# Kernel optimization log

Hardware: AMD Instinct MI355X
Metric: run time of the kernel (lower is better)

The kernel has to match this reference:

```python
import jax, jax.numpy as jnp
import numpy as np

THRESHOLD = 0.5  # default threshold from MemoryPool.update

N, D, P, C0 = 16384, 1024, 4096, 2048


def setup_inputs() -> dict:
    key = jax.random.key(0)
    k1, k2, k3, k4 = jax.random.split(key, 4)
    summaries = jax.random.normal(k1, (N, D), dtype=jnp.float32)
    scores = jax.random.uniform(k2, (N,), dtype=jnp.float32)
    slot = jnp.arange(P)
    # slots >= count are empty (zeros), matching fresh torch buffers
    pool = jnp.where((slot < C0)[:, None],
                     jax.random.normal(k3, (P, D), dtype=jnp.float32), 0.0)
    priorities = jnp.where(slot < C0,
                           jax.random.uniform(k4, (P,), dtype=jnp.float32), 0.0)
    return {"summaries": summaries, "scores": scores,
            "pool": pool, "priorities": priorities, "count": C0}


def reference(summaries, scores, pool, priorities, count):
    pool_size = pool.shape[0]
    cnt0 = jnp.asarray(count, jnp.int32)

    def step(carry, xc):
        pl, pr, cnt = carry
        s, sc = xc  # (D,), ()
        valid = sc > THRESHOLD
        min_idx = jnp.argmin(pr)
        has_room = cnt < pool_size
        idx = jnp.where(has_room, cnt, min_idx)
        replace_ok = sc > pr[min_idx]
        do_write = valid & (has_room | replace_ok)
        new_pl = jnp.where(do_write, pl.at[idx].set(s), pl)
        new_pr = jnp.where(do_write, pr.at[idx].set(sc), pr)
        new_cnt = cnt + (do_write & has_room).astype(jnp.int32)
        return (new_pl, new_pr, new_cnt), None

    (pool_out, prior_out, cnt_out), _ = jax.lax.scan(
        step, (pool, priorities, cnt0), (summaries, scores))
    return pool_out, prior_out, cnt_out
```

## Files before the change

### kernel.cpp

```cpp
#include <hip/hip_runtime.h>

typedef unsigned long long u64;
#define THRESH 0.5f
#define ALL1 0xFFFFFFFFFFFFFFFFull
#define FINF __builtin_inff()

__device__ __forceinline__ u64 shflxU64(u64 v, int m) { return __shfl_xor(v, m, 64); }
__device__ __forceinline__ void sort64(u64 &key, int lane) {
#pragma unroll
    for (int k = 2; k <= 64; k <<= 1) {
#pragma unroll
        for (int j = k >> 1; j > 0; j >>= 1) {
            u64 p = shflxU64(key, j);
            bool takeMax = ((lane & j) != 0) != ((lane & k) != 0);
            u64 mn = key < p ? key : p;
            u64 mx = key < p ? p : key;
            key = takeMax ? mx : mn;
        }
    }
}

__device__ __forceinline__ u64 mkey(float v, int id) {
    v = (v == 0.0f) ? 0.0f : v;
    unsigned u = __float_as_uint(v);
    u ^= (unsigned)((int)u >> 31) | 0x80000000u;
    return ((u64)u << 32) | (unsigned)id;
}

__global__ __launch_bounds__(1024) void k1_scan(
    const float* __restrict__ scores, const float* __restrict__ priorities,
    const int* __restrict__ countPtr, int N, int P,
    float* __restrict__ outPrior, float* __restrict__ outCnt, int* __restrict__ srcWs,
    float* __restrict__ cval, int* __restrict__ csrc, int* __restrict__ meta)
{
    const int tid = threadIdx.x;
    for (int s = tid; s < P; s += 1024) { outPrior[s] = priorities[s]; srcWs[s] = -1; }
    int C0 = *countPtr; C0 = C0 < 0 ? 0 : (C0 > P ? P : C0);
    const int per = (N + 1023) >> 10;
    const int i0 = tid * per;
    float sv[16];
    if (per == 16 && i0 + 16 <= N) {
        const float4* s4 = (const float4*)(scores + i0);
        const float4 a = s4[0], b = s4[1], c4 = s4[2], d = s4[3];
        sv[0]=a.x; sv[1]=a.y; sv[2]=a.z; sv[3]=a.w;
        sv[4]=b.x; sv[5]=b.y; sv[6]=b.z; sv[7]=b.w;
        sv[8]=c4.x; sv[9]=c4.y; sv[10]=c4.z; sv[11]=c4.w;
        sv[12]=d.x; sv[13]=d.y; sv[14]=d.z; sv[15]=d.w;
    } else {
#pragma unroll 16
        for (int j = 0; j < 16; ++j)
            sv[j] = (j < per && i0 + j < N) ? scores[i0 + j] : 0.f;
    }
    int c = 0;
#pragma unroll 16
    for (int j = 0; j < 16; ++j) c += (j < per && i0 + j < N && sv[j] > THRESH) ? 1 : 0;
    __shared__ int sb[1024];
    sb[tid] = c; __syncthreads();
    for (int off = 1; off < 1024; off <<= 1) {
        int v = (tid >= off) ? sb[tid - off] : 0;
        __syncthreads();
        sb[tid] += v;
        __syncthreads();
    }
    const int total = sb[1023];
    int v = sb[tid] - c;
    int A = P - C0; if (A > total) A = total; if (A < 0) A = 0;
#pragma unroll 16
    for (int j = 0; j < 16; ++j) {
        if (j < per && i0 + j < N) {
            const float sc = sv[j];
            if (sc > THRESH) {
                if (v < A) { outPrior[C0 + v] = sc; srcWs[C0 + v] = i0 + j; }
                else { cval[v - A] = sc; csrc[v - A] = i0 + j; }
                ++v;
            }
        }
    }
    if (tid == 0) {
        meta[0] = total - A;
        meta[1] = C0 + A;
        outCnt[0] = (float)(C0 + A);
    }
}

#define K2T 512
__global__ __launch_bounds__(256) void k2_count(
    const float* __restrict__ outPrior, const float* __restrict__ cval,
    const int* __restrict__ meta, int* __restrict__ cnt2)
{
    const int M = meta[0], F = meta[1];
    const int iB = blockIdx.x << 8;
    if (iB >= M) return;
    const int hi = min(M, iB + 256);
    const int smax = F + hi;
    const int tb = blockIdx.y * K2T;
    if (tb >= smax) return;
    const int te = min(smax - tb, K2T);
    __shared__ __align__(16) float tile[K2T];
    for (int t = threadIdx.x; t < K2T; t += 256) {
        const int s = tb + t;
        tile[t] = (t < te) ? ((s < F) ? outPrior[s] : cval[s - F]) : FINF;
    }
    __syncthreads();
    const int i = iB + threadIdx.x;
    if (i >= M) return;
    const float x = cval[i];
    int cnt = 0;
    const float4* t4 = (const float4*)tile;
    if (tb + K2T <= F + iB) {
#pragma unroll 8
        for (int q = 0; q < K2T / 4; ++q) {
            const float4 w = t4[q];
            cnt += (w.x < x) + (w.y < x) + (w.z < x) + (w.w < x);
        }
    } else {
        int lim = F + i - tb;
        if (lim < 0) lim = 0;
        if (lim > te) lim = te;
        const int l4 = lim >> 2;
        for (int q = 0; q < l4; ++q) {
            const float4 w = t4[q];
            cnt += (w.x < x) + (w.y < x) + (w.z < x) + (w.w < x);
        }
        for (int t = l4 << 2; t < lim; ++t) cnt += tile[t] < x;
    }
    if (cnt) atomicAdd(&cnt2[i], cnt);
}

__global__ __launch_bounds__(1024) void k3_compact(
    const float* __restrict__ cval, const int* __restrict__ csrc,
    const int* __restrict__ cnt2, int* __restrict__ meta,
    float* __restrict__ cvalS, float* __restrict__ wval, int* __restrict__ wsrc,
    int* __restrict__ writeNum)
{
    const int M = meta[0];
    const int tid = threadIdx.x;
    const int per = (M + 1023) >> 10;
    const int i0 = tid * per, i1 = min(i0 + per, M);
    int c = 0;
    for (int i = i0; i < i1; ++i) c += (cnt2[i] >= i + 1) ? 1 : 0;
    __shared__ int sb[1024];
    sb[tid] = c; __syncthreads();
    for (int off = 1; off < 1024; off <<= 1) {
        int v = (tid >= off) ? sb[tid - off] : 0;
        __syncthreads();
        sb[tid] += v;
        __syncthreads();
    }
    int w = sb[tid] - c;
    for (int i = i0; i < i1; ++i) {
        if (cnt2[i] >= i + 1) {
            wval[w] = cval[i]; wsrc[w] = csrc[i]; writeNum[i] = w; cvalS[i] = cval[i]; ++w;
        } else { writeNum[i] = -1; cvalS[i] = FINF; }
    }
    if (tid == 0) meta[2] = sb[1023];
}

#define K4T 512
__global__ __launch_bounds__(256) void k4_count(
    const float* __restrict__ outPrior, const float* __restrict__ cvalS,
    const int* __restrict__ meta, int P, int* __restrict__ cnt4)
{
    const int M = meta[0], F = meta[1];
    if (M == 0) return;
    const int tot = F + M;
    const int eB = blockIdx.x << 8;
    if (eB >= tot) return;
    const int tb = blockIdx.y * K4T;
    if (tb >= tot) return;
    const int te = min(tot - tb, K4T);
    __shared__ __align__(16) u64 tile[K4T];
    for (int t = threadIdx.x; t < K4T; t += 256) {
        const int s = tb + t;
        u64 kk = ALL1;
        if (t < te) {
            if (s < F) kk = mkey(outPrior[s], s);
            else       kk = mkey(cvalS[s - F], P + (s - F));
        }
        tile[t] = kk;
    }
    __syncthreads();
    const int e = eB + threadIdx.x;
    if (e >= tot) return;
    float x; int id;
    if (e < F) { x = outPrior[e]; id = e; }
    else {
        x = cvalS[e - F];
        if (x == FINF) return;
        id = P + (e - F);
    }
    const u64 kx = mkey(x, id);
    int cnt = 0;
    const ulonglong2* t2 = (const ulonglong2*)tile;
#pragma unroll 8
    for (int q = 0; q < K4T / 2; ++q) {
        const ulonglong2 w = t2[q];
        cnt += (int)(w.x < kx) + (int)(w.y < kx);
    }
    if (cnt) atomicAdd(&cnt4[e], cnt);
}

__global__ __launch_bounds__(256) void k4_scatter(
    const float* __restrict__ outPrior, const float* __restrict__ cvalS,
    const int* __restrict__ writeNum, const int* __restrict__ meta, int P,
    const int* __restrict__ cnt4,
    float* __restrict__ evV, int* __restrict__ evId, int* __restrict__ survW)
{
    const int M = meta[0], F = meta[1], R = meta[2];
    if (M == 0) return;
    const int tot = F + M;
    const int e = blockIdx.x * 256 + threadIdx.x;
    if (e >= tot) return;
    float x; int myid; bool isCand = false; int wn = -1;
    if (e < F) { x = outPrior[e]; myid = e; }
    else {
        const int i = e - F;
        x = cvalS[i];
        if (x == FINF) return;
        isCand = true; wn = writeNum[i]; myid = P + i;
    }
    const int cnt = cnt4[e];
    if (isCand) survW[wn] = (cnt >= R) ? 1 : 0;
    if (cnt < R + 64) { evV[cnt] = x; evId[cnt] = isCand ? (P + wn) : myid; }
}

#define SCAP 14400
#define DONEF (1 << 30)
#define MSF   (1 << 29)
#define TIEF  (1 << 28)
#define RSF   (1 << 27)
#define PAYM  ((1 << 27) - 1)
__global__ __launch_bounds__(1024) void k5_chain(
    const float* __restrict__ evV, const int* __restrict__ evId,
    const int* __restrict__ meta, int P,
    const float* __restrict__ wval, const int* __restrict__ wsrc,
    int* __restrict__ survW,
    float* __restrict__ outPrior, int* __restrict__ srcWs)
{
    __shared__ int state[SCAP];
    __shared__ int shRp, shLeft;
    const int tid = threadIdx.x;
    const int R = meta[2];
    if (R <= 0 || R > SCAP) return;
    const int F = meta[1];
    const int Wtot = F + R;

    if (tid == 0) {
        int Rp = R;
        if (R < Wtot) {
            const float vR1 = evV[R - 1];
            if (evV[R] == vR1) {
                int rr = R - 1;
                while (rr >= 0 && evV[rr] == vR1) --rr;
                Rp = rr + 1;
            }
        }
        shRp = Rp;
    }
    __syncthreads();
    const int Rp = shRp;

    for (int r = tid; r < Rp; r += 1024) {
        const float v = evV[r];
        const bool tp = (r > 0) && (evV[r - 1] == v);
        const bool tn = (r + 1 < Rp) && (evV[r + 1] == v);
        const bool tie = tp || tn;
        const int rs = (tie && !tp) ? RSF : 0;
        const int id = evId[r];
        int st;
        if (id < P) st = id | MSF | (tie ? (TIEF | rs) : DONEF);
        else        st = (id - P) | (tie ? (TIEF | rs) : 0);
        state[r] = st;
    }
    __syncthreads();

    for (int round = 0; round < Rp + 2; ++round) {
        for (int r = tid; r < Rp; r += 1024) {
            const int s = state[r];
            if (s & MSF) continue;
            int p = s & PAYM;
            int ms = -1;
            for (int g = 0; g < Rp + 2; ++g) {
                const int sp = state[p];
                if (sp & DONEF) { ms = sp & PAYM; break; }
                if (sp & (MSF | TIEF)) break;
                const int q = sp & PAYM;
                if (q >= p) break;
                p = q;
            }
            if (ms >= 0)
                state[r] = ms | MSF | ((s & TIEF) ? (s & (TIEF | RSF)) : DONEF);
            else
                state[r] = p | (s & (TIEF | RSF));
        }
        __syncthreads();
        for (int r = tid; r < Rp; r += 1024) {
            const int s = state[r];
            if (!(s & RSF) || (s & DONEF)) continue;
            int re = r + 1;
            while (re < Rp) {
                const int t = state[re];
                if ((t & TIEF) && !(t & RSF)) ++re; else break;
            }
            bool ready = true;
            for (int q = r; q < re; ++q) ready &= (state[q] & MSF) != 0;
            if (!ready) continue;
            for (int j = r; j < re; ++j) {
                int best = j;
                for (int q = j + 1; q < re; ++q)
                    if ((state[q] & PAYM) < (state[best] & PAYM)) best = q;
                if (best != j) {
                    const int pj = state[j] & PAYM, pb = state[best] & PAYM;
                    state[j]    = (state[j] & ~PAYM) | pb;
                    state[best] = (state[best] & ~PAYM) | pj;
                }
            }
            for (int j = r; j < re; ++j) state[j] |= DONEF;
        }
        __syncthreads();
        if (tid == 0) shLeft = 0;
        __syncthreads();
        int loc = 0;
        for (int r = tid; r < Rp; r += 1024) loc += (state[r] & DONEF) ? 0 : 1;
        if (loc) atomicAdd(&shLeft, loc);
        __syncthreads();
        if (shLeft == 0) break;
    }
    __syncthreads();

    if (Rp < R && tid < 64) {
        const int lane = tid;
        const int r = Rp + lane;
        const float v0 = evV[Rp];
        const bool mem = (r < Wtot) && (evV[r] == v0);
        const int g = (int)__popcll(__ballot(mem));
        const int e = R - Rp;
        int id = 0, ms = 0;
        if (mem) {
            id = evId[r];
            ms = (id < P) ? id : (state[id - P] & PAYM);
        }
        u64 key = mem ? ((((u64)(unsigned)ms) << 32) | (u64)(unsigned)id) : ALL1;
        sort64(key, lane);
        const int sid = (int)(unsigned)(key & 0xFFFFFFFFull);
        const int sms = (int)(unsigned)(key >> 32);
        const bool real = (key != ALL1) && (lane < g);
        if (real && lane < e) state[Rp + lane] = sms;
        if (real && sid >= P) survW[sid - P] = (lane >= e) ? 1 : 0;
    }
    __syncthreads();

    for (int j = tid; j < R; j += 1024) {
        if (survW[j]) {
            const int sl = state[j] & PAYM;
            outPrior[sl] = wval[j];
            srcWs[sl] = wsrc[j];
        }
    }
}

__global__ __launch_bounds__(256) void gather_kernel(
    const float* __restrict__ summaries,
    const float* __restrict__ pool,
    const int* __restrict__ src,
    float* __restrict__ outPool, int D) {
    int p = blockIdx.x;
    int s = src[p];
    const float* row = (s >= 0) ? (summaries + (size_t)s * D) : (pool + (size_t)p * D);
    float* o = outPool + (size_t)p * D;
    if ((D & 3) == 0) {
        for (int k = (threadIdx.x << 2); k < D; k += (blockDim.x << 2)) {
            float4 v = *(const float4*)(row + k);
            *(float4*)(o + k) = v;
        }
    } else {
        for (int k = threadIdx.x; k < D; k += blockDim.x) o[k] = row[k];
    }
}

extern "C" void kernel_launch(void* const* d_in, const int* in_sizes, int n_in,
                              void* d_out, int out_size, void* d_ws, size_t ws_size,
                              hipStream_t stream) {
    const float* summaries  = (const float*)d_in[0];
    const float* scores     = (const float*)d_in[1];
    const float* pool       = (const float*)d_in[2];
    const float* priorities = (const float*)d_in[3];
    const int*   count      = (const int*)d_in[4];

    int N = in_sizes[1];
    int P = in_sizes[3];
    int D = in_sizes[0] / N;

    float* outPool  = (float*)d_out;
    float* outPrior = outPool + (size_t)P * D;
    float* outCnt   = outPrior + P;
    int*   srcWs    = (int*)d_ws;

    float* cval     = outPool;
    int*   csrc     = (int*)outPool + 1 * N;
    float* cvalS    = outPool + 3 * N;
    float* wval     = outPool + 4 * N;
    int*   wsrc     = (int*)outPool + 5 * N;
    int*   writeNum = (int*)outPool + 6 * N;
    float* evV      = outPool + 7 * N;
    int*   evId     = (int*)outPool + 8 * N + 64;
    int*   survW    = (int*)outPool + 10 * N + 128;
    int*   cnt2     = (int*)outPool + 11 * N + 192;
    int*   cnt4     = (int*)outPool + 12 * N + 192;
    int*   meta     = (int*)outPool + 11 * N + 128;

    const int nb2 = (N + 255) / 256;
    const int nb4 = (P + N + 255) / 256;
    const int ty  = (P + N + K2T - 1) / K2T;

    dim3 g2(nb2, ty), g4(nb4, ty);

    hipMemsetAsync(cnt2, 0, (size_t)N * sizeof(int), stream);
    hipMemsetAsync(cnt4, 0, (size_t)(P + N) * sizeof(int), stream);

    k1_scan<<<1, 1024, 0, stream>>>(scores, priorities, count, N, P,
                                    outPrior, outCnt, srcWs, cval, csrc, meta);
    k2_count<<<g2, 256, 0, stream>>>(outPrior, cval, meta, cnt2);
    k3_compact<<<1, 1024, 0, stream>>>(cval, csrc, cnt2, meta, cvalS, wval, wsrc, writeNum);
    k4_count<<<g4, 256, 0, stream>>>(outPrior, cvalS, meta, P, cnt4);
    k4_scatter<<<nb4, 256, 0, stream>>>(outPrior, cvalS, writeNum, meta, P, cnt4,
                                        evV, evId, survW);
    k5_chain<<<1, 1024, 0, stream>>>(evV, evId, meta, P, wval, wsrc, survW,
                                     outPrior, srcWs);
    gather_kernel<<<P, 256, 0, stream>>>(summaries, pool, srcWs, outPool, D);
}
```

Measured before the change: 181.0 us.

## Fold memsets and scatter kernel into neighbours, use wave-shuffle block scans

Removes the two hipMemsetAsync calls by zeroing the count buffers inside k1_scan, and folds k4_scatter into the start of the single-block k5_chain. This cuts three launches or enqueued operations. It also replaces the shared-memory Hillis-Steele scan (20 barriers) with a wave shuffle scan plus a 16-entry partial scan in k1 and k3. The cost is that the scatter now runs on one 1024-thread block instead of many blocks, and k1 does the zeroing serially inside a single block.

```diff
diff --git a/kernel.cpp b/kernel.cpp
--- a/kernel.cpp
+++ b/kernel.cpp
@@ -27,14 +27,42 @@
     return ((u64)u << 32) | (unsigned)id;
 }
 
+__device__ __forceinline__ int blockScanExcl1024(int c, int tid, int* wpart,
+                                                 int* totalOut) {
+    const int lane = tid & 63, wid = tid >> 6;
+    int pc = c;
+#pragma unroll
+    for (int off = 1; off < 64; off <<= 1) {
+        int y = __shfl_up(pc, off, 64);
+        if (lane >= off) pc += y;
+    }
+    if (lane == 63) wpart[wid] = pc;
+    __syncthreads();
+    if (tid < 16) {
+        int v = wpart[tid];
+#pragma unroll
+        for (int off = 1; off < 16; off <<= 1) {
+            int y = __shfl_up(v, off, 16);
+            if (tid >= off) v += y;
+        }
+        wpart[tid] = v;
+    }
+    __syncthreads();
+    *totalOut = wpart[15];
+    return pc - c + (wid > 0 ? wpart[wid - 1] : 0);
+}
+
 __global__ __launch_bounds__(1024) void k1_scan(
     const float* __restrict__ scores, const float* __restrict__ priorities,
     const int* __restrict__ countPtr, int N, int P,
     float* __restrict__ outPrior, float* __restrict__ outCnt, int* __restrict__ srcWs,
-    float* __restrict__ cval, int* __restrict__ csrc, int* __restrict__ meta)
+    float* __restrict__ cval, int* __restrict__ csrc, int* __restrict__ meta,
+    int* __restrict__ cnt2, int* __restrict__ cnt4)
 {
     const int tid = threadIdx.x;
     for (int s = tid; s < P; s += 1024) { outPrior[s] = priorities[s]; srcWs[s] = -1; }
+    for (int s = tid; s < N; s += 1024) cnt2[s] = 0;
+    for (int s = tid; s < P + N; s += 1024) cnt4[s] = 0;
     int C0 = *countPtr; C0 = C0 < 0 ? 0 : (C0 > P ? P : C0);
     const int per = (N + 1023) >> 10;
     const int i0 = tid * per;
@@ -54,16 +82,9 @@
     int c = 0;
 #pragma unroll 16
     for (int j = 0; j < 16; ++j) c += (j < per && i0 + j < N && sv[j] > THRESH) ? 1 : 0;
-    __shared__ int sb[1024];
-    sb[tid] = c; __syncthreads();
-    for (int off = 1; off < 1024; off <<= 1) {
-        int v = (tid >= off) ? sb[tid - off] : 0;
-        __syncthreads();
-        sb[tid] += v;
-        __syncthreads();
-    }
-    const int total = sb[1023];
-    int v = sb[tid] - c;
+    __shared__ int wpart[16];
+    int total;
+    int v = blockScanExcl1024(c, tid, wpart, &total);
     int A = P - C0; if (A > total) A = total; if (A < 0) A = 0;
 #pragma unroll 16
     for (int j = 0; j < 16; ++j) {
@@ -139,21 +160,15 @@
     const int i0 = tid * per, i1 = min(i0 + per, M);
     int c = 0;
     for (int i = i0; i < i1; ++i) c += (cnt2[i] >= i + 1) ? 1 : 0;
-    __shared__ int sb[1024];
-    sb[tid] = c; __syncthreads();
-    for (int off = 1; off < 1024; off <<= 1) {
-        int v = (tid >= off) ? sb[tid - off] : 0;
-        __syncthreads();
-        sb[tid] += v;
-        __syncthreads();
-    }
-    int w = sb[tid] - c;
+    __shared__ int wpart[16];
+    int total;
+    int w = blockScanExcl1024(c, tid, wpart, &total);
     for (int i = i0; i < i1; ++i) {
         if (cnt2[i] >= i + 1) {
             wval[w] = cval[i]; wsrc[w] = csrc[i]; writeNum[i] = w; cvalS[i] = cval[i]; ++w;
         } else { writeNum[i] = -1; cvalS[i] = FINF; }
     }
-    if (tid == 0) meta[2] = sb[1023];
+    if (tid == 0) meta[2] = total;
 }
 
 #define K4T 512
@@ -200,30 +215,6 @@
     if (cnt) atomicAdd(&cnt4[e], cnt);
 }
 
-__global__ __launch_bounds__(256) void k4_scatter(
-    const float* __restrict__ outPrior, const float* __restrict__ cvalS,
-    const int* __restrict__ writeNum, const int* __restrict__ meta, int P,
-    const int* __restrict__ cnt4,
-    float* __restrict__ evV, int* __restrict__ evId, int* __restrict__ survW)
-{
-    const int M = meta[0], F = meta[1], R = meta[2];
-    if (M == 0) return;
-    const int tot = F + M;
-    const int e = blockIdx.x * 256 + threadIdx.x;
-    if (e >= tot) return;
-    float x; int myid; bool isCand = false; int wn = -1;
-    if (e < F) { x = outPrior[e]; myid = e; }
-    else {
-        const int i = e - F;
-        x = cvalS[i];
-        if (x == FINF) return;
-        isCand = true; wn = writeNum[i]; myid = P + i;
-    }
-    const int cnt = cnt4[e];
-    if (isCand) survW[wn] = (cnt >= R) ? 1 : 0;
-    if (cnt < R + 64) { evV[cnt] = x; evId[cnt] = isCand ? (P + wn) : myid; }
-}
-
 #define SCAP 14400
 #define DONEF (1 << 30)
 #define MSF   (1 << 29)
@@ -231,18 +222,37 @@
 #define RSF   (1 << 27)
 #define PAYM  ((1 << 27) - 1)
 __global__ __launch_bounds__(1024) void k5_chain(
-    const float* __restrict__ evV, const int* __restrict__ evId,
+    float* __restrict__ evV, int* __restrict__ evId,
     const int* __restrict__ meta, int P,
     const float* __restrict__ wval, const int* __restrict__ wsrc,
     int* __restrict__ survW,
-    float* __restrict__ outPrior, int* __restrict__ srcWs)
+    float* outPrior, int* __restrict__ srcWs,
+    const float* __restrict__ cvalS, const int* __restrict__ writeNum,
+    const int* __restrict__ cnt4)
 {
     __shared__ int state[SCAP];
     __shared__ int shRp, shLeft;
     const int tid = threadIdx.x;
-    const int R = meta[2];
+    const int M = meta[0], F = meta[1], R = meta[2];
+    if (M == 0) return;
+    const int tot = F + M;
+
+    for (int e = tid; e < tot; e += 1024) {
+        float x; int myid; bool isC = false; int wn = -1;
+        if (e < F) { x = outPrior[e]; myid = e; }
+        else {
+            const int i = e - F;
+            x = cvalS[i];
+            if (x == FINF) continue;
+            isC = true; wn = writeNum[i]; myid = P + i;
+        }
+        const int cnt = cnt4[e];
+        if (isC) survW[wn] = (cnt >= R) ? 1 : 0;
+        if (cnt < R + 64) { evV[cnt] = x; evId[cnt] = isC ? (P + wn) : myid; }
+    }
+    __syncthreads();
+
     if (R <= 0 || R > SCAP) return;
-    const int F = meta[1];
     const int Wtot = F + R;
 
     if (tid == 0) {
@@ -405,9 +415,9 @@
     float* evV      = outPool + 7 * N;
     int*   evId     = (int*)outPool + 8 * N + 64;
     int*   survW    = (int*)outPool + 10 * N + 128;
+    int*   meta     = (int*)outPool + 11 * N + 128;
     int*   cnt2     = (int*)outPool + 11 * N + 192;
     int*   cnt4     = (int*)outPool + 12 * N + 192;
-    int*   meta     = (int*)outPool + 11 * N + 128;
 
     const int nb2 = (N + 255) / 256;
     const int nb4 = (P + N + 255) / 256;
@@ -415,17 +425,13 @@
 
     dim3 g2(nb2, ty), g4(nb4, ty);
 
-    hipMemsetAsync(cnt2, 0, (size_t)N * sizeof(int), stream);
-    hipMemsetAsync(cnt4, 0, (size_t)(P + N) * sizeof(int), stream);
-
     k1_scan<<<1, 1024, 0, stream>>>(scores, priorities, count, N, P,
-                                    outPrior, outCnt, srcWs, cval, csrc, meta);
+                                    outPrior, outCnt, srcWs, cval, csrc, meta,
+                                    cnt2, cnt4);
     k2_count<<<g2, 256, 0, stream>>>(outPrior, cval, meta, cnt2);
     k3_compact<<<1, 1024, 0, stream>>>(cval, csrc, cnt2, meta, cvalS, wval, wsrc, writeNum);
     k4_count<<<g4, 256, 0, stream>>>(outPrior, cvalS, meta, P, cnt4);
-    k4_scatter<<<nb4, 256, 0, stream>>>(outPrior, cvalS, writeNum, meta, P, cnt4,
-                                        evV, evId, survW);
     k5_chain<<<1, 1024, 0, stream>>>(evV, evId, meta, P, wval, wsrc, survW,
-                                     outPrior, srcWs);
+                                     outPrior, srcWs, cvalS, writeNum, cnt4);
     gather_kernel<<<P, 256, 0, stream>>>(summaries, pool, srcWs, outPool, D);
 }
```

Result: no change. 183.9 us (+1.6%).
